# Performance work log

Hardware: AMD Instinct MI355X
Metric: run time of the kernel (lower is better)

The kernel has to match this reference:

```python
import jax, jax.numpy as jnp
from jax import lax
import numpy as np
import math

B, C, Hs, Ws = 2, 512, 48, 48
HW = Hs * Ws            # 2304; also m (compress_ratio = 1)
M = HW
GROUPS = 256
GS = M // GROUPS        # 9, exact split
ALPHA = 0.05
MAXITER = 43
TOL = B * HW * 1e-7     # torch: z0.numel()*tol with z0 of shape [N, HW]
EPS = 1e-5
POWER_ITERS = 100


def _make_A():
    # random projection: num_ones = round(sqrt(m)) ones per column, rows L2-normalized
    rng = np.random.RandomState(0)
    num_ones = int(round(math.sqrt(M)))  # 48
    A = np.zeros((M, HW), dtype=np.float32)
    rows = np.argsort(rng.rand(HW, M), axis=1)[:, :num_ones]  # [HW, num_ones]
    A[rows.ravel(), np.repeat(np.arange(HW), num_ones)] = 1.0
    A /= np.maximum(np.sqrt((A ** 2).sum(axis=1, keepdims=True)), 1e-12)
    return jnp.asarray(A)


def setup_inputs() -> dict:
    key = jax.random.key(0)
    ks = jax.random.split(key, 10)
    f32 = jnp.float32
    d = {
        'content': jax.random.normal(ks[0], (B, C, Hs, Ws), f32),
        'style': jax.random.normal(ks[1], (B, C, Hs, Ws), f32),
        'content_key': jax.random.normal(ks[2], (B, C, Hs, Ws), f32),
        'style_key': jax.random.normal(ks[3], (B, C, Hs, Ws), f32),
        'f_w': jax.random.normal(ks[4], (C, C), f32) * 0.02,
        'f_b': jnp.zeros((C,), f32),
        'g_w': jax.random.normal(ks[5], (C, C), f32) * 0.02,
        'g_b': jnp.zeros((C,), f32),
        'h_w': jax.random.normal(ks[6], (C, C), f32) * 0.02,
        'h_b': jnp.zeros((C,), f32),
        'A': _make_A(),
    }
    return d


def _conv1x1(x, w, b):
    # nn.Conv2d(Cin, Cout, 1): [b,c,h,w] x [o,c] + bias
    return jnp.einsum('bchw,oc->bohw', x, w) + b[None, :, None, None]


def _softshrink(x, lam):
    return jnp.sign(x) * jnp.maximum(jnp.abs(x) - lam, 0.0)


def _forward(content, style, content_key, style_key, f_w, f_b, g_w, g_b, h_w, h_b, A):
    Fq = _conv1x1(content_key, f_w, f_b).reshape(B, C, HW).transpose(0, 2, 1)  # [b,HWc,Ck]
    G = _conv1x1(style_key, g_w, g_b).reshape(B, C, HW)                        # [b,Ck,HWs]
    Hh = _conv1x1(style, h_w, h_b).reshape(B, C, HW)
    # HW <= max_sample: no subsampling branch
    style_flat = Hh.transpose(0, 2, 1)                                         # [b,HWs,C]
    S = jax.nn.softmax(jnp.einsum('bqc,bck->bqk', Fq, G), axis=-1)             # [b,HWc,HWs]
    mean = jnp.einsum('bqk,bkc->bqc', S, style_flat)                           # weighted mean
    std = jnp.sqrt(jax.nn.relu(jnp.einsum('bqk,bkc->bqc', S, style_flat ** 2) - mean ** 2))
    mean = mean.transpose(0, 2, 1)  # [b,C,HW]
    std = std.transpose(0, 2, 1)
    # random projection along spatial dim: feat @ A^T
    proj = lambda f: jnp.einsum('mh,bch->bcm', A, f)
    mean_c = proj(mean)
    std_c = proj(std)
    cont_c = proj(content.reshape(B, C, HW))
    # per-group mean/variance norm (256 equal groups of GS along compressed dim)
    g = cont_c.reshape(B, C, GROUPS, GS)
    mu = g.mean(axis=-1, keepdims=True)
    var = g.var(axis=-1, ddof=1, keepdims=True)  # torch var is unbiased
    normed = (g - mu) / jnp.sqrt(var + EPS)
    x = (normed * std_c.reshape(B, C, GROUPS, GS)
         + mean_c.reshape(B, C, GROUPS, GS)).reshape(B, C, M)
    # FISTA sparse coding: min 0.5||z A^T - x||^2 + alpha |z|_1
    Ad = lax.stop_gradient(A)
    WtW = Ad.T @ Ad
    v = jnp.full((HW,), 1.0 / math.sqrt(HW), jnp.float32)
    def _pi(v, _):
        w = WtW @ v
        return w / jnp.linalg.norm(w), None
    v, _ = lax.scan(_pi, v, None, length=POWER_ITERS)
    L = v @ (WtW @ v)  # largest eigenvalue of A^T A
    lr = 1.0 / L
    z0 = jnp.zeros((B, C, HW), x.dtype)

    def step(carry, _):
        z, y, t, done = carry
        resid = jnp.einsum('bch,mh->bcm', y, A) - x   # y @ A^T - x
        grad = jnp.einsum('bcm,mh->bch', resid, A)    # resid @ A
        zn = _softshrink(y - lr * grad, ALPHA * lr)
        diff = jnp.abs(z - zn).sum()
        tn = (1.0 + jnp.sqrt(1.0 + 4.0 * t * t)) / 2.0
        yn = zn + (t - 1.0) / tn * (zn - z)
        z2 = jnp.where(done, z, zn)
        y2 = jnp.where(done, y, yn)
        t2 = jnp.where(done, t, tn)
        done2 = done | (diff <= TOL)
        return (z2, y2, t2, done2), None

    (z, _, _, _), _ = lax.scan(step, (z0, z0, jnp.float32(1.0), jnp.array(False)),
                               None, length=MAXITER)
    return z.reshape(B, C, Hs, Ws)


def reference(content, style, content_key, style_key, f_w, f_b, g_w, g_b, h_w, h_b, A):
    return _forward(content, style, content_key, style_key,
                    f_w, f_b, g_w, g_b, h_w, h_b, A)
```

## Files before the change

### kernel.cpp

```cpp
#include <hip/hip_runtime.h>
#include <math.h>

#define TPB 256

typedef _Float16 f16;
typedef _Float16 half8 __attribute__((ext_vector_type(8)));
typedef _Float16 f16x2 __attribute__((ext_vector_type(2)));
typedef _Float16 f16x4 __attribute__((ext_vector_type(4)));
typedef float floatx4 __attribute__((ext_vector_type(4)));

static constexpr int CDIM = 512;
static constexpr int HWD = 2304;
static constexpr float ALPHA = 0.05f;
static constexpr float TOLF = 4.608e-4f;

enum { EPI_F32 = 0, EPI_F16BIASN = 1, EPI_F16BIASM = 2, EPI_F16 = 3,
       EPI_WTW = 4, EPI_MEANSTD = 5, EPI_FISTA = 6 };

__device__ __forceinline__ bool fista_done(const float* __restrict__ diffArr, int iter) {
    bool done = false;
    for (int j = 0; j < iter; ++j) done = done || (diffArr[j] <= TOLF);
    return done;
}

__device__ __forceinline__ void gload_lds(const f16* g, f16* l) {
#if __has_builtin(__builtin_amdgcn_global_load_lds)
    __builtin_amdgcn_global_load_lds(
        (__attribute__((address_space(1))) void*)(g),
        (__attribute__((address_space(3))) void*)(l), 16, 0, 0);
#else
    *(int4*)l = *(const int4*)g;
#endif
}

template<int N> __device__ __forceinline__ void vwait() {
    if constexpr (N == 0)      asm volatile("s_waitcnt vmcnt(0)" ::: "memory");
    else if constexpr (N == 3) asm volatile("s_waitcnt vmcnt(3)" ::: "memory");
    else if constexpr (N == 4) asm volatile("s_waitcnt vmcnt(4)" ::: "memory");
}

__device__ __forceinline__ void barrier_f() {
    asm volatile("" ::: "memory");
    __builtin_amdgcn_s_barrier();
    asm volatile("" ::: "memory");
}

template<int EPI, int MF>
__global__ __launch_bounds__(TPB, 4) void sgemm(
    const f16* __restrict__ A, long a_bs, int lda,
    const f16* __restrict__ B, long b_bs, int ldb,
    void* __restrict__ C0, long c_bs, int ldc,
    void* __restrict__ C1,
    int K,
    const float* __restrict__ bias,
    const float* __restrict__ xAf,
    float* __restrict__ zc, float* __restrict__ zp, f16* __restrict__ yhp,
    const float* __restrict__ lrs, float coefPrev, float coefCur,
    float* __restrict__ diffArr, int iter)
{
    if (EPI == EPI_FISTA) {
        if (iter > 0 && fista_done(diffArr, iter)) return;
    }
    constexpr int ASZ = MF * 32 * 64;
    constexpr int BSZ = 64 * 64;
    constexpr int LCNT = MF + 2;
    __shared__ alignas(16) f16 As[2 * ASZ];
    __shared__ alignas(16) f16 Bs[2 * BSZ];
    const int tid = threadIdx.x;
    const int wid = tid >> 6, lane = tid & 63;
    const int wr = wid >> 1, wc = wid & 1;

    const int gx = gridDim.x, gy = gridDim.y;
    const int nwg = gx * gy;
    const int d = blockIdx.y * gx + blockIdx.x;
    const int q = nwg >> 3, r = nwg & 7;
    const int xcd = d & 7, rest = d >> 3;
    const int wgid = (xcd < r ? xcd * (q + 1) : r * (q + 1) + (xcd - r) * q) + rest;
    const int bx = wgid / gy, by = wgid % gy;

    const int m0 = by * (MF * 32), n0 = bx << 6;
    const f16* Ab = A + (long)blockIdx.z * a_bs;
    const f16* Bb = B + (long)blockIdx.z * b_bs;

    floatx4 acc[MF][2] = {};
    floatx4 acc2[MF][2] = {};

    const int rl = lane & 15, kg = lane >> 4;
    const int lrow = lane >> 3;
    const int gs = (lane & 7) ^ lrow;

    const int nt = K >> 6;

    auto STAGE = [&](int t, int buf) {
        const long k0 = (long)t << 6;
        f16* Ad = As + buf * ASZ;
        f16* Bd = Bs + buf * BSZ;
        #pragma unroll
        for (int p = 0; p < MF; ++p) {
            const int c = wid * MF + p;
            const int R = c * 8 + lrow;
            gload_lds(Ab + (long)(m0 + R) * lda + k0 + gs * 8, Ad + c * 512);
        }
        #pragma unroll
        for (int p = 0; p < 2; ++p) {
            const int c = wid * 2 + p;
            const int R = c * 8 + lrow;
            gload_lds(Bb + (long)(n0 + R) * ldb + k0 + gs * 8, Bd + c * 512);
        }
    };

    STAGE(0, 0);
    for (int t = 0; t < nt; ++t) {
        if (t + 1 < nt) {
            STAGE(t + 1, (t + 1) & 1);
            vwait<LCNT>();
        } else {
            vwait<0>();
        }
        barrier_f();
        const f16* Ac = As + (t & 1) * ASZ;
        const f16* Bc = Bs + (t & 1) * BSZ;
        #pragma unroll
        for (int kk = 0; kk < 2; ++kk) {
            const int j = kk * 4 + kg;
            half8 af[MF], bf[2];
            #pragma unroll
            for (int f = 0; f < MF; ++f) {
                const int rowa = wr * (MF * 16) + f * 16 + rl;
                af[f] = *(const half8*)&Ac[rowa * 64 + ((j ^ (rowa & 7)) * 8)];
            }
            #pragma unroll
            for (int f = 0; f < 2; ++f) {
                const int rowb = wc * 32 + f * 16 + rl;
                bf[f] = *(const half8*)&Bc[rowb * 64 + ((j ^ (rowb & 7)) * 8)];
            }
            #pragma unroll
            for (int fi = 0; fi < MF; ++fi) {
                #pragma unroll
                for (int fj = 0; fj < 2; ++fj) {
                    acc[fi][fj] = __builtin_amdgcn_mfma_f32_16x16x32_f16(af[fi], bf[fj], acc[fi][fj], 0, 0, 0);
                    if constexpr (EPI == EPI_MEANSTD) {
                        half8 bq = bf[fj] * bf[fj];
                        acc2[fi][fj] = __builtin_amdgcn_mfma_f32_16x16x32_f16(af[fi], bq, acc2[fi][fj], 0, 0, 0);
                    }
                }
            }
        }
        barrier_f();
    }

    const int rg = lane >> 4;
    const int bz = blockIdx.z;
    float loc = 0.f;
    float lr = 0.f, sh = 0.f;
    if constexpr (EPI == EPI_FISTA) { lr = lrs[0]; sh = lrs[1]; }

    #pragma unroll
    for (int fi = 0; fi < MF; ++fi) {
        #pragma unroll
        for (int fj = 0; fj < 2; ++fj) {
            #pragma unroll
            for (int r2 = 0; r2 < 4; ++r2) {
                const int row = m0 + wr * (MF * 16) + fi * 16 + rg * 4 + r2;
                const int col = n0 + wc * 32 + fj * 16 + rl;
                const float v = acc[fi][fj][r2];
                if constexpr (EPI == EPI_F32) {
                    ((float*)C0)[bz * c_bs + (long)row * ldc + col] = v;
                } else if constexpr (EPI == EPI_F16BIASN) {
                    ((f16*)C0)[bz * c_bs + (long)row * ldc + col] = (f16)(v + bias[col]);
                } else if constexpr (EPI == EPI_F16BIASM) {
                    ((f16*)C0)[bz * c_bs + (long)row * ldc + col] = (f16)(v + bias[row]);
                } else if constexpr (EPI == EPI_F16) {
                    ((f16*)C0)[bz * c_bs + (long)row * ldc + col] = (f16)v;
                } else if constexpr (EPI == EPI_WTW) {
                    ((float*)C0)[(long)row * ldc + col] = v;
                    ((f16*)C1)[(long)row * ldc + col] = (f16)v;
                } else if constexpr (EPI == EPI_MEANSTD) {
                    const float m_ = v;
                    float s2 = acc2[fi][fj][r2] - m_ * m_;
                    const long o = ((long)bz * CDIM + col) * HWD + row;
                    ((f16*)C0)[o] = (f16)m_;
                    ((f16*)C1)[o] = (f16)sqrtf(s2 > 0.f ? s2 : 0.f);
                } else {
                    const long off = (long)row * HWD + col;
                    const float zk = zc[off];
                    const float zkm = zp[off];
                    const float ykf = zk + coefPrev * (zk - zkm);
                    const float grad = v - xAf[off];
                    const float p = ykf - lr * grad;
                    const float ap = fabsf(p) - sh;
                    const float zn = ap > 0.f ? copysignf(ap, p) : 0.f;
                    zp[off] = zn;
                    yhp[off] = (f16)(zn + coefCur * (zn - zk));
                    loc += fabsf(zn - zk);
                }
            }
        }
    }
    if constexpr (EPI == EPI_FISTA) {
        __shared__ float red[TPB];
        red[tid] = loc; __syncthreads();
        for (int s = 128; s > 0; s >>= 1) { if (tid < s) red[tid] += red[tid + s]; __syncthreads(); }
        if (tid == 0) atomicAdd(&diffArr[iter], red[0]);
    }
}

__global__ __launch_bounds__(TPB) void tcvt(const float* __restrict__ in, long in_bs,
                                            f16* __restrict__ out, long out_bs, int R, int Cc) {
    __shared__ float t[32][33];
    const int b = blockIdx.z;
    const int r0 = blockIdx.y << 5, c0 = blockIdx.x << 5;
    const int tx = threadIdx.x & 31, ty = threadIdx.x >> 5;
    const float* ib = in + (long)b * in_bs;
    #pragma unroll
    for (int p = 0; p < 4; ++p) {
        const int r = ty + p * 8;
        t[r][tx] = ib[(long)(r0 + r) * Cc + c0 + tx];
    }
    __syncthreads();
    f16* ob = out + (long)b * out_bs;
    #pragma unroll
    for (int p = 0; p < 4; ++p) {
        const int c = ty + p * 8;
        ob[(long)(c0 + c) * R + r0 + tx] = (f16)t[tx][c];
    }
}

__global__ void cvt16(const float4* __restrict__ in, f16x4* __restrict__ out, long n4) {
    long i = (long)blockIdx.x * blockDim.x + threadIdx.x;
    const long st = (long)gridDim.x * blockDim.x;
    for (; i < n4; i += st) {
        const float4 v = in[i];
        f16x4 o; o.x = (f16)v.x; o.y = (f16)v.y; o.z = (f16)v.z; o.w = (f16)v.w;
        out[i] = o;
    }
}

__global__ __launch_bounds__(TPB) void softmax_h(const float* __restrict__ Sf, f16* __restrict__ Sh) {
    __shared__ float row[HWD];
    __shared__ float red[TPB];
    const long base = (long)blockIdx.x * HWD;
    const int tid = threadIdx.x;
    float mx = -3.4e38f;
    for (int i = tid; i < HWD; i += TPB) { const float v = Sf[base + i]; row[i] = v; mx = fmaxf(mx, v); }
    red[tid] = mx; __syncthreads();
    for (int s = 128; s > 0; s >>= 1) { if (tid < s) red[tid] = fmaxf(red[tid], red[tid + s]); __syncthreads(); }
    mx = red[0]; __syncthreads();
    float sum = 0.f;
    for (int i = tid; i < HWD; i += TPB) { const float e = expf(row[i] - mx); row[i] = e; sum += e; }
    red[tid] = sum; __syncthreads();
    for (int s = 128; s > 0; s >>= 1) { if (tid < s) red[tid] += red[tid + s]; __syncthreads(); }
    const float inv = 1.0f / red[0];
    for (int i = tid; i < HWD; i += TPB) Sh[base + i] = (f16)(row[i] * inv);
}

__global__ __launch_bounds__(TPB) void groupnorm_x(const float* __restrict__ contc,
                                                   const float* __restrict__ meanc,
                                                   const float* __restrict__ stdc,
                                                   f16* __restrict__ xh) {
    const long base = (long)blockIdx.x * HWD + (long)threadIdx.x * 9;
    float v[9];
    float mu = 0.f;
    #pragma unroll
    for (int j = 0; j < 9; ++j) { v[j] = contc[base + j]; mu += v[j]; }
    mu *= (1.0f / 9.0f);
    float var = 0.f;
    #pragma unroll
    for (int j = 0; j < 9; ++j) { const float d = v[j] - mu; var += d * d; }
    var *= (1.0f / 8.0f);
    const float rs = 1.0f / sqrtf(var + 1e-5f);
    #pragma unroll
    for (int j = 0; j < 9; ++j)
        xh[base + j] = (f16)((v[j] - mu) * rs * (float)stdc[base + j] + (float)meanc[base + j]);
}

__global__ __launch_bounds__(TPB) void matvec_h(const f16* __restrict__ Wm,
                                                const float* __restrict__ win,
                                                float* __restrict__ wout) {
    __shared__ float red[TPB];
    const int tid = threadIdx.x;
    float s = 0.f;
    for (int i = tid; i < HWD; i += TPB) { const float v = win[i]; s += v * v; }
    red[tid] = s; __syncthreads();
    for (int st = 128; st > 0; st >>= 1) { if (tid < st) red[tid] += red[tid + st]; __syncthreads(); }
    const float ninv = rsqrtf(red[0]);
    const int row = (blockIdx.x << 2) + (tid >> 6);
    const int lane = tid & 63;
    const f16x2* wr2 = (const f16x2*)(Wm + (long)row * HWD);
    float d = 0.f;
    for (int j = lane; j < HWD / 2; j += 64) {
        const f16x2 p = wr2[j];
        d += (float)p.x * win[2 * j] + (float)p.y * win[2 * j + 1];
    }
    #pragma unroll
    for (int o = 32; o > 0; o >>= 1) d += __shfl_down(d, o);
    if (lane == 0) wout[row] = d * ninv;
}

__global__ __launch_bounds__(TPB) void kernelL(const float* __restrict__ Wf,
                                               const float* __restrict__ w,
                                               float* __restrict__ Lnum, float* __restrict__ Lden) {
    __shared__ float red[TPB];
    const int tid = threadIdx.x;
    const int row = (blockIdx.x << 2) + (tid >> 6);
    const int lane = tid & 63;
    const float* wr = Wf + (long)row * HWD;
    float d = 0.f;
    for (int j = lane; j < HWD; j += 64) d += wr[j] * w[j];
    #pragma unroll
    for (int o = 32; o > 0; o >>= 1) d += __shfl_down(d, o);
    red[tid] = (lane == 0) ? d * w[row] : 0.f;
    __syncthreads();
    for (int s = 128; s > 0; s >>= 1) { if (tid < s) red[tid] += red[tid + s]; __syncthreads(); }
    if (tid == 0) atomicAdd(Lnum, red[0]);
    if (blockIdx.x == 0) {
        __syncthreads();
        float s2 = 0.f;
        for (int i = tid; i < HWD; i += TPB) { const float v = w[i]; s2 += v * v; }
        red[tid] = s2; __syncthreads();
        for (int s = 128; s > 0; s >>= 1) { if (tid < s) red[tid] += red[tid + s]; __syncthreads(); }
        if (tid == 0) *Lden = red[0];
    }
}

__global__ void lr_fin(const float* __restrict__ Lnum, const float* __restrict__ Lden,
                       float* __restrict__ lrs) {
    const float lr = Lden[0] / Lnum[0];
    lrs[0] = lr;
    lrs[1] = ALPHA * lr;
}

__global__ void init_small(float* __restrict__ wvec, float* __restrict__ diffArr,
                           float* __restrict__ Lnum) {
    const int tid = threadIdx.x;
    for (int i = tid; i < HWD; i += TPB) wvec[i] = (float)(1.0 / 48.0);
    if (tid < 43) diffArr[tid] = 0.f;
    if (tid == 64) Lnum[0] = 0.f;
}

__global__ void zero_kernel(float4* __restrict__ p, long n4) {
    long i = (long)blockIdx.x * blockDim.x + threadIdx.x;
    const long st = (long)gridDim.x * blockDim.x;
    for (; i < n4; i += st) p[i] = make_float4(0.f, 0.f, 0.f, 0.f);
}

__global__ void copy_fista(const float4* __restrict__ zfA, const float4* __restrict__ zfB,
                           float4* __restrict__ out, const float* __restrict__ diffArr, long n4) {
    int last = 42;
    for (int j = 0; j < 43; ++j) { if (diffArr[j] <= TOLF) { last = j; break; } }
    const float4* src = (last & 1) ? zfA : zfB;
    long i = (long)blockIdx.x * blockDim.x + threadIdx.x;
    const long st = (long)gridDim.x * blockDim.x;
    for (; i < n4; i += st) out[i] = src[i];
}

extern "C" void kernel_launch(void* const* d_in, const int* in_sizes, int n_in,
                              void* d_out, int out_size, void* d_ws, size_t ws_size,
                              hipStream_t stream) {
    (void)in_sizes; (void)n_in; (void)out_size;
    const float* content = (const float*)d_in[0];
    const float* style   = (const float*)d_in[1];
    const float* ckey    = (const float*)d_in[2];
    const float* skey    = (const float*)d_in[3];
    const float* f_w = (const float*)d_in[4];
    const float* f_b = (const float*)d_in[5];
    const float* g_w = (const float*)d_in[6];
    const float* g_b = (const float*)d_in[7];
    const float* h_w = (const float*)d_in[8];
    const float* h_b = (const float*)d_in[9];
    const float* Amat = (const float*)d_in[10];

    if (ws_size < 79500000) return;
    char* W = (char*)d_ws;

    const long E16 = (long)HWD * CDIM;
    const long EHH = (long)HWD * HWD;
    f16*  ckeyT = (f16*)(W + 0);
    f16*  skeyT = (f16*)(W + 4718592);
    f16*  styleT= (f16*)(W + 9437184);
    float* Sf   = (float*)(W + 0);
    f16*  Ah    = (f16*)(W + 0);
    f16*  At    = (f16*)(W + 10616832);
    f16*  Wh    = (f16*)(W + 21233664);
    f16*  W4h   = (f16*)(W + 31850496);
    f16*  W2h   = (f16*)(W + 0);
    float* contc= (float*)(W + 21233664);
    float* zfA  = (float*)(W + 0);
    float* zfB  = (float*)(W + 9437184);
    f16*  yh    = (f16*)(W + 31850496);
    f16*  Sh    = (f16*)(W + 42467328);
    float* meanc= (float*)(W + 42467328);
    float* stdc = (float*)(W + 42467328 + 9437184);
    float* Wf   = (float*)(W + 42467328);
    float* xAf  = (float*)(W + 42467328);
    f16*  Fh    = (f16*)(W + 63700992);
    f16*  Gh    = (f16*)(W + 63700992 + 4718592);
    f16*  Hh    = (f16*)(W + 63700992 + 9437184);
    f16*  meanx = (f16*)(W + 63700992);
    f16*  stdx  = (f16*)(W + 63700992 + 4718592);
    f16*  conth = (f16*)(W + 63700992 + 9437184);
    f16*  xh    = (f16*)(W + 63700992);
    float* w_a  = (float*)(W + 77856768);
    float* w_b  = (float*)(W + 77856768 + 9216);
    float* lrs  = (float*)(W + 77856768 + 18432);
    float* Lnum = (float*)(W + 77856768 + 18440);
    float* Lden = (float*)(W + 77856768 + 18444);
    float* diffArr = (float*)(W + 77856768 + 18448);
    f16*  fwh   = (f16*)(W + 77875712);
    f16*  gwh   = (f16*)(W + 77875712 + 524288);
    f16*  hwh   = (f16*)(W + 77875712 + 1048576);

    init_small<<<1, TPB, 0, stream>>>(w_a, diffArr, Lnum);

    cvt16<<<256, TPB, 0, stream>>>((const float4*)f_w, (f16x4*)fwh, (long)CDIM * CDIM / 4);
    cvt16<<<256, TPB, 0, stream>>>((const float4*)g_w, (f16x4*)gwh, (long)CDIM * CDIM / 4);
    cvt16<<<256, TPB, 0, stream>>>((const float4*)h_w, (f16x4*)hwh, (long)CDIM * CDIM / 4);
    tcvt<<<dim3(72, 16, 2), TPB, 0, stream>>>(ckey, E16, ckeyT, E16, CDIM, HWD);
    tcvt<<<dim3(72, 16, 2), TPB, 0, stream>>>(skey, E16, skeyT, E16, CDIM, HWD);
    tcvt<<<dim3(72, 16, 2), TPB, 0, stream>>>(style, E16, styleT, E16, CDIM, HWD);

    sgemm<EPI_F16BIASN, 1><<<dim3(8, 72, 2), TPB, 0, stream>>>(ckeyT, E16, CDIM, fwh, 0, CDIM,
        Fh, E16, CDIM, nullptr, CDIM, f_b, nullptr, nullptr, nullptr, nullptr, nullptr, 0.f, 0.f, nullptr, 0);
    sgemm<EPI_F16BIASN, 1><<<dim3(8, 72, 2), TPB, 0, stream>>>(skeyT, E16, CDIM, gwh, 0, CDIM,
        Gh, E16, CDIM, nullptr, CDIM, g_b, nullptr, nullptr, nullptr, nullptr, nullptr, 0.f, 0.f, nullptr, 0);
    sgemm<EPI_F16BIASM, 1><<<dim3(36, 16, 2), TPB, 0, stream>>>(hwh, 0, CDIM, styleT, E16, CDIM,
        Hh, E16, HWD, nullptr, CDIM, h_b, nullptr, nullptr, nullptr, nullptr, nullptr, 0.f, 0.f, nullptr, 0);

    sgemm<EPI_F32, 2><<<dim3(36, 36, 2), TPB, 0, stream>>>(Fh, E16, CDIM, Gh, E16, CDIM,
        Sf, EHH, HWD, nullptr, CDIM, nullptr, nullptr, nullptr, nullptr, nullptr, nullptr, 0.f, 0.f, nullptr, 0);
    softmax_h<<<2 * HWD, TPB, 0, stream>>>(Sf, Sh);

    cvt16<<<2048, TPB, 0, stream>>>((const float4*)Amat, (f16x4*)Ah, EHH / 4);
    tcvt<<<dim3(72, 72, 1), TPB, 0, stream>>>(Amat, 0, At, 0, HWD, HWD);

    sgemm<EPI_MEANSTD, 1><<<dim3(8, 72, 2), TPB, 0, stream>>>(Sh, EHH, HWD, Hh, E16, HWD,
        meanx, 0, HWD, stdx, HWD, nullptr, nullptr, nullptr, nullptr, nullptr, nullptr, 0.f, 0.f, nullptr, 0);

    cvt16<<<2048, TPB, 0, stream>>>((const float4*)content, (f16x4*)conth, (long)2 * E16 / 4);

    sgemm<EPI_F32, 1><<<dim3(36, 32, 1), TPB, 0, stream>>>(meanx, 0, HWD, Ah, 0, HWD,
        meanc, 0, HWD, nullptr, HWD, nullptr, nullptr, nullptr, nullptr, nullptr, nullptr, 0.f, 0.f, nullptr, 0);
    sgemm<EPI_F32, 1><<<dim3(36, 32, 1), TPB, 0, stream>>>(stdx, 0, HWD, Ah, 0, HWD,
        stdc, 0, HWD, nullptr, HWD, nullptr, nullptr, nullptr, nullptr, nullptr, nullptr, 0.f, 0.f, nullptr, 0);
    sgemm<EPI_F32, 1><<<dim3(36, 32, 1), TPB, 0, stream>>>(conth, 0, HWD, Ah, 0, HWD,
        contc, 0, HWD, nullptr, HWD, nullptr, nullptr, nullptr, nullptr, nullptr, nullptr, 0.f, 0.f, nullptr, 0);

    groupnorm_x<<<1024, TPB, 0, stream>>>(contc, meanc, stdc, xh);

    sgemm<EPI_WTW, 2><<<dim3(36, 36, 1), TPB, 0, stream>>>(At, 0, HWD, At, 0, HWD,
        Wf, 0, HWD, Wh, HWD, nullptr, nullptr, nullptr, nullptr, nullptr, nullptr, 0.f, 0.f, nullptr, 0);
    sgemm<EPI_F16, 2><<<dim3(36, 36, 1), TPB, 0, stream>>>(Wh, 0, HWD, Wh, 0, HWD,
        W2h, 0, HWD, nullptr, HWD, nullptr, nullptr, nullptr, nullptr, nullptr, nullptr, 0.f, 0.f, nullptr, 0);
    sgemm<EPI_F16, 2><<<dim3(36, 36, 1), TPB, 0, stream>>>(W2h, 0, HWD, W2h, 0, HWD,
        W4h, 0, HWD, nullptr, HWD, nullptr, nullptr, nullptr, nullptr, nullptr, nullptr, 0.f, 0.f, nullptr, 0);

    for (int it = 0; it < 25; ++it) {
        const float* win = (it & 1) ? w_b : w_a;
        float* wout = (it & 1) ? w_a : w_b;
        matvec_h<<<HWD / 4, TPB, 0, stream>>>(W4h, win, wout);
    }
    kernelL<<<HWD / 4, TPB, 0, stream>>>(Wf, w_b, Lnum, Lden);
    lr_fin<<<1, 1, 0, stream>>>(Lnum, Lden, lrs);

    sgemm<EPI_F32, 1><<<dim3(36, 32, 1), TPB, 0, stream>>>(xh, 0, HWD, At, 0, HWD,
        xAf, 0, HWD, nullptr, HWD, nullptr, nullptr, nullptr, nullptr, nullptr, nullptr, 0.f, 0.f, nullptr, 0);

    zero_kernel<<<1024, TPB, 0, stream>>>((float4*)zfA, E16);
    zero_kernel<<<1024, TPB, 0, stream>>>((float4*)yh, E16 / 4);

    float t = 1.0f, coefPrev = 0.0f;
    for (int it = 0; it < 43; ++it) {
        const float tn = (1.0f + sqrtf(1.0f + 4.0f * t * t)) * 0.5f;
        const float coef = (t - 1.0f) / tn;
        t = tn;
        float* zc = (it & 1) ? zfB : zfA;
        float* zp = (it & 1) ? zfA : zfB;
        sgemm<EPI_FISTA, 1><<<dim3(36, 32, 1), TPB, 0, stream>>>(yh, 0, HWD, Wh, 0, HWD,
            nullptr, 0, HWD, nullptr, HWD, nullptr, xAf, zc, zp, yh, lrs, coefPrev, coef, diffArr, it);
        coefPrev = coef;
    }

    copy_fista<<<2048, TPB, 0, stream>>>((const float4*)zfA, (const float4*)zfB,
                                         (float4*)d_out, diffArr, 2 * E16 / 4);
}
```

Baseline: 2.423 ms.

## Run FISTA loop as one persistent cooperative kernel with register-resident state

Replaces the 43 separate FISTA GEMM launches with a single cooperative persistent kernel. It keeps z, y and xA in registers, ping-pongs y between two fp16 buffers, and uses a grid-wide sync plus an atomic diff sum for early exit. The aim is to remove launch overhead and the z/zp global-memory traffic each iteration. Other GEMMs move to larger M tiles (MF=2) to cut launch counts and reuse B tiles. The change adds grid.sync cost and relies on all 288 blocks being co-resident, falling back to a per-step kernel otherwise.

```diff
diff --git a/kernel.cpp b/kernel.cpp
--- a/kernel.cpp
+++ b/kernel.cpp
@@ -1,5 +1,8 @@
 #include <hip/hip_runtime.h>
+#include <hip/hip_cooperative_groups.h>
 #include <math.h>
+
+namespace cg = cooperative_groups;
 
 #define TPB 256
 
@@ -15,7 +18,7 @@
 static constexpr float TOLF = 4.608e-4f;
 
 enum { EPI_F32 = 0, EPI_F16BIASN = 1, EPI_F16BIASM = 2, EPI_F16 = 3,
-       EPI_WTW = 4, EPI_MEANSTD = 5, EPI_FISTA = 6 };
+       EPI_WTW = 4, EPI_MEANSTD = 5 };
 
 __device__ __forceinline__ bool fista_done(const float* __restrict__ diffArr, int iter) {
     bool done = false;
@@ -35,8 +38,8 @@
 
 template<int N> __device__ __forceinline__ void vwait() {
     if constexpr (N == 0)      asm volatile("s_waitcnt vmcnt(0)" ::: "memory");
-    else if constexpr (N == 3) asm volatile("s_waitcnt vmcnt(3)" ::: "memory");
     else if constexpr (N == 4) asm volatile("s_waitcnt vmcnt(4)" ::: "memory");
+    else if constexpr (N == 6) asm volatile("s_waitcnt vmcnt(6)" ::: "memory");
 }
 
 __device__ __forceinline__ void barrier_f() {
@@ -52,15 +55,8 @@
     void* __restrict__ C0, long c_bs, int ldc,
     void* __restrict__ C1,
     int K,
-    const float* __restrict__ bias,
-    const float* __restrict__ xAf,
-    float* __restrict__ zc, float* __restrict__ zp, f16* __restrict__ yhp,
-    const float* __restrict__ lrs, float coefPrev, float coefCur,
-    float* __restrict__ diffArr, int iter)
+    const float* __restrict__ bias)
 {
-    if (EPI == EPI_FISTA) {
-        if (iter > 0 && fista_done(diffArr, iter)) return;
-    }
     constexpr int ASZ = MF * 32 * 64;
     constexpr int BSZ = 64 * 64;
     constexpr int LCNT = MF + 2;
@@ -88,7 +84,6 @@
     const int rl = lane & 15, kg = lane >> 4;
     const int lrow = lane >> 3;
     const int gs = (lane & 7) ^ lrow;
-
     const int nt = K >> 6;
 
     auto STAGE = [&](int t, int buf) {
@@ -111,12 +106,8 @@
 
     STAGE(0, 0);
     for (int t = 0; t < nt; ++t) {
-        if (t + 1 < nt) {
-            STAGE(t + 1, (t + 1) & 1);
-            vwait<LCNT>();
-        } else {
-            vwait<0>();
-        }
+        if (t + 1 < nt) { STAGE(t + 1, (t + 1) & 1); vwait<LCNT>(); }
+        else            { vwait<0>(); }
         barrier_f();
         const f16* Ac = As + (t & 1) * ASZ;
         const f16* Bc = Bs + (t & 1) * BSZ;
@@ -151,10 +142,6 @@
 
     const int rg = lane >> 4;
     const int bz = blockIdx.z;
-    float loc = 0.f;
-    float lr = 0.f, sh = 0.f;
-    if constexpr (EPI == EPI_FISTA) { lr = lrs[0]; sh = lrs[1]; }
-
     #pragma unroll
     for (int fi = 0; fi < MF; ++fi) {
         #pragma unroll
@@ -181,28 +168,262 @@
                     const long o = ((long)bz * CDIM + col) * HWD + row;
                     ((f16*)C0)[o] = (f16)m_;
                     ((f16*)C1)[o] = (f16)sqrtf(s2 > 0.f ? s2 : 0.f);
-                } else {
-                    const long off = (long)row * HWD + col;
-                    const float zk = zc[off];
-                    const float zkm = zp[off];
-                    const float ykf = zk + coefPrev * (zk - zkm);
-                    const float grad = v - xAf[off];
-                    const float p = ykf - lr * grad;
+                }
+            }
+        }
+    }
+}
+
+__global__ __launch_bounds__(TPB, 2) void fista_coop(
+    const f16* __restrict__ Wh,
+    const float* __restrict__ xAf,
+    f16* __restrict__ yA, f16* __restrict__ yB,
+    const float* __restrict__ lrs,
+    float* __restrict__ diffArr,
+    float* __restrict__ dout)
+{
+    cg::grid_group grid = cg::this_grid();
+    constexpr int MF = 4;
+    constexpr int ASZ = MF * 32 * 64;
+    constexpr int BSZ = 64 * 64;
+    constexpr int LCNT = MF + 2;
+    __shared__ alignas(16) f16 As[2 * ASZ];
+    __shared__ alignas(16) f16 Bs[2 * BSZ];
+    __shared__ float red[TPB];
+    const int tid = threadIdx.x;
+    const int wid = tid >> 6, lane = tid & 63;
+    const int wr = wid >> 1, wc = wid & 1;
+
+    const int d = blockIdx.x;
+    const int wgid = (d & 7) * 36 + (d >> 3);
+    const int bx = wgid >> 3, by = wgid & 7;
+    const int m0 = by << 7, n0 = bx << 6;
+
+    const int rl = lane & 15, kg = lane >> 4;
+    const int rg = lane >> 4;
+    const int lrow = lane >> 3;
+    const int gs = (lane & 7) ^ lrow;
+    constexpr int nt = HWD >> 6;
+
+    const float lr = lrs[0], sh = lrs[1];
+
+    float xar[MF][2][4], zr[MF][2][4], yr[MF][2][4];
+    #pragma unroll
+    for (int fi = 0; fi < MF; ++fi)
+        #pragma unroll
+        for (int fj = 0; fj < 2; ++fj)
+            #pragma unroll
+            for (int r2 = 0; r2 < 4; ++r2) {
+                const int row = m0 + wr * (MF * 16) + fi * 16 + rg * 4 + r2;
+                const int col = n0 + wc * 32 + fj * 16 + rl;
+                xar[fi][fj][r2] = xAf[(long)row * HWD + col];
+                zr[fi][fj][r2] = 0.f;
+                yr[fi][fj][r2] = 0.f;
+            }
+
+    float t = 1.0f;
+    for (int iter = 0; iter < 43; ++iter) {
+        const float tn = (1.0f + sqrtf(1.0f + 4.0f * t * t)) * 0.5f;
+        const float coef = (t - 1.0f) / tn;
+        t = tn;
+        const f16* Yin = (iter & 1) ? yB : yA;
+        f16* Yout = (iter & 1) ? yA : yB;
+
+        floatx4 acc[MF][2] = {};
+        auto STAGE = [&](int tt, int buf) {
+            const long k0 = (long)tt << 6;
+            f16* Ad = As + buf * ASZ;
+            f16* Bd = Bs + buf * BSZ;
+            #pragma unroll
+            for (int p = 0; p < MF; ++p) {
+                const int c = wid * MF + p;
+                const int R = c * 8 + lrow;
+                gload_lds(Yin + (long)(m0 + R) * HWD + k0 + gs * 8, Ad + c * 512);
+            }
+            #pragma unroll
+            for (int p = 0; p < 2; ++p) {
+                const int c = wid * 2 + p;
+                const int R = c * 8 + lrow;
+                gload_lds(Wh + (long)(n0 + R) * HWD + k0 + gs * 8, Bd + c * 512);
+            }
+        };
+        STAGE(0, 0);
+        for (int tt = 0; tt < nt; ++tt) {
+            if (tt + 1 < nt) { STAGE(tt + 1, (tt + 1) & 1); vwait<LCNT>(); }
+            else             { vwait<0>(); }
+            barrier_f();
+            const f16* Ac = As + (tt & 1) * ASZ;
+            const f16* Bc = Bs + (tt & 1) * BSZ;
+            #pragma unroll
+            for (int kk = 0; kk < 2; ++kk) {
+                const int j = kk * 4 + kg;
+                half8 af[MF], bf[2];
+                #pragma unroll
+                for (int f = 0; f < MF; ++f) {
+                    const int rowa = wr * (MF * 16) + f * 16 + rl;
+                    af[f] = *(const half8*)&Ac[rowa * 64 + ((j ^ (rowa & 7)) * 8)];
+                }
+                #pragma unroll
+                for (int f = 0; f < 2; ++f) {
+                    const int rowb = wc * 32 + f * 16 + rl;
+                    bf[f] = *(const half8*)&Bc[rowb * 64 + ((j ^ (rowb & 7)) * 8)];
+                }
+                #pragma unroll
+                for (int fi = 0; fi < MF; ++fi)
+                    #pragma unroll
+                    for (int fj = 0; fj < 2; ++fj)
+                        acc[fi][fj] = __builtin_amdgcn_mfma_f32_16x16x32_f16(af[fi], bf[fj], acc[fi][fj], 0, 0, 0);
+            }
+            barrier_f();
+        }
+
+        float loc = 0.f;
+        #pragma unroll
+        for (int fi = 0; fi < MF; ++fi)
+            #pragma unroll
+            for (int fj = 0; fj < 2; ++fj)
+                #pragma unroll
+                for (int r2 = 0; r2 < 4; ++r2) {
+                    const int row = m0 + wr * (MF * 16) + fi * 16 + rg * 4 + r2;
+                    const int col = n0 + wc * 32 + fj * 16 + rl;
+                    const float grad = acc[fi][fj][r2] - xar[fi][fj][r2];
+                    const float p = yr[fi][fj][r2] - lr * grad;
                     const float ap = fabsf(p) - sh;
                     const float zn = ap > 0.f ? copysignf(ap, p) : 0.f;
-                    zp[off] = zn;
-                    yhp[off] = (f16)(zn + coefCur * (zn - zk));
-                    loc += fabsf(zn - zk);
+                    const float zo = zr[fi][fj][r2];
+                    loc += fabsf(zn - zo);
+                    const float yn = zn + coef * (zn - zo);
+                    zr[fi][fj][r2] = zn;
+                    yr[fi][fj][r2] = yn;
+                    Yout[(long)row * HWD + col] = (f16)yn;
                 }
-            }
-        }
-    }
-    if constexpr (EPI == EPI_FISTA) {
-        __shared__ float red[TPB];
         red[tid] = loc; __syncthreads();
         for (int s = 128; s > 0; s >>= 1) { if (tid < s) red[tid] += red[tid + s]; __syncthreads(); }
         if (tid == 0) atomicAdd(&diffArr[iter], red[0]);
-    }
+
+        __threadfence();
+        grid.sync();
+        __threadfence();
+        const float dsum = __hip_atomic_load(&diffArr[iter], __ATOMIC_RELAXED,
+                                             __HIP_MEMORY_SCOPE_AGENT);
+        if (dsum <= TOLF) break;
+    }
+
+    #pragma unroll
+    for (int fi = 0; fi < MF; ++fi)
+        #pragma unroll
+        for (int fj = 0; fj < 2; ++fj)
+            #pragma unroll
+            for (int r2 = 0; r2 < 4; ++r2) {
+                const int row = m0 + wr * (MF * 16) + fi * 16 + rg * 4 + r2;
+                const int col = n0 + wc * 32 + fj * 16 + rl;
+                dout[(long)row * HWD + col] = zr[fi][fj][r2];
+            }
+}
+
+__global__ __launch_bounds__(TPB, 3) void fista_step(
+    const f16* __restrict__ Yin, const f16* __restrict__ Wh,
+    const float* __restrict__ xAf,
+    float* __restrict__ zc, float* __restrict__ zp, f16* __restrict__ yhp,
+    const float* __restrict__ lrs, float coefPrev, float coefCur,
+    float* __restrict__ diffArr, int iter)
+{
+    if (iter > 0 && fista_done(diffArr, iter)) return;
+    constexpr int MF = 2;
+    constexpr int ASZ = MF * 32 * 64;
+    constexpr int BSZ = 64 * 64;
+    constexpr int LCNT = MF + 2;
+    __shared__ alignas(16) f16 As[2 * ASZ];
+    __shared__ alignas(16) f16 Bs[2 * BSZ];
+    __shared__ float red[TPB];
+    const int tid = threadIdx.x;
+    const int wid = tid >> 6, lane = tid & 63;
+    const int wr = wid >> 1, wc = wid & 1;
+
+    const int d = blockIdx.y * gridDim.x + blockIdx.x;
+    const int wgid = (d & 7) * 72 + (d >> 3);
+    const int bx = wgid >> 4, by = wgid & 15;
+    const int m0 = by << 6, n0 = bx << 6;
+
+    floatx4 acc[MF][2] = {};
+    const int rl = lane & 15, kg = lane >> 4;
+    const int lrow = lane >> 3;
+    const int gs = (lane & 7) ^ lrow;
+    constexpr int nt = HWD >> 6;
+
+    auto STAGE = [&](int t, int buf) {
+        const long k0 = (long)t << 6;
+        f16* Ad = As + buf * ASZ;
+        f16* Bd = Bs + buf * BSZ;
+        #pragma unroll
+        for (int p = 0; p < MF; ++p) {
+            const int c = wid * MF + p;
+            const int R = c * 8 + lrow;
+            gload_lds(Yin + (long)(m0 + R) * HWD + k0 + gs * 8, Ad + c * 512);
+        }
+        #pragma unroll
+        for (int p = 0; p < 2; ++p) {
+            const int c = wid * 2 + p;
+            const int R = c * 8 + lrow;
+            gload_lds(Wh + (long)(n0 + R) * HWD + k0 + gs * 8, Bd + c * 512);
+        }
+    };
+    STAGE(0, 0);
+    for (int t = 0; t < nt; ++t) {
+        if (t + 1 < nt) { STAGE(t + 1, (t + 1) & 1); vwait<LCNT>(); }
+        else            { vwait<0>(); }
+        barrier_f();
+        const f16* Ac = As + (t & 1) * ASZ;
+        const f16* Bc = Bs + (t & 1) * BSZ;
+        #pragma unroll
+        for (int kk = 0; kk < 2; ++kk) {
+            const int j = kk * 4 + kg;
+            half8 af[MF], bf[2];
+            #pragma unroll
+            for (int f = 0; f < MF; ++f) {
+                const int rowa = wr * (MF * 16) + f * 16 + rl;
+                af[f] = *(const half8*)&Ac[rowa * 64 + ((j ^ (rowa & 7)) * 8)];
+            }
+            #pragma unroll
+            for (int f = 0; f < 2; ++f) {
+                const int rowb = wc * 32 + f * 16 + rl;
+                bf[f] = *(const half8*)&Bc[rowb * 64 + ((j ^ (rowb & 7)) * 8)];
+            }
+            #pragma unroll
+            for (int fi = 0; fi < MF; ++fi)
+                #pragma unroll
+                for (int fj = 0; fj < 2; ++fj)
+                    acc[fi][fj] = __builtin_amdgcn_mfma_f32_16x16x32_f16(af[fi], bf[fj], acc[fi][fj], 0, 0, 0);
+        }
+        barrier_f();
+    }
+
+    const int rg = lane >> 4;
+    const float lr = lrs[0], sh = lrs[1];
+    float loc = 0.f;
+    #pragma unroll
+    for (int fi = 0; fi < MF; ++fi)
+        #pragma unroll
+        for (int fj = 0; fj < 2; ++fj)
+            #pragma unroll
+            for (int r2 = 0; r2 < 4; ++r2) {
+                const int row = m0 + wr * (MF * 16) + fi * 16 + rg * 4 + r2;
+                const int col = n0 + wc * 32 + fj * 16 + rl;
+                const long off = (long)row * HWD + col;
+                const float zk = zc[off];
+                const float zkm = zp[off];
+                const float ykf = zk + coefPrev * (zk - zkm);
+                const float grad = acc[fi][fj][r2] - xAf[off];
+                const float p = ykf - lr * grad;
+                const float ap = fabsf(p) - sh;
+                const float zn = ap > 0.f ? copysignf(ap, p) : 0.f;
+                zp[off] = zn;
+                yhp[off] = (f16)(zn + coefCur * (zn - zk));
+                loc += fabsf(zn - zk);
+            }
+    red[tid] = loc; __syncthreads();
+    for (int s = 128; s > 0; s >>= 1) { if (tid < s) red[tid] += red[tid + s]; __syncthreads(); }
+    if (tid == 0) atomicAdd(&diffArr[iter], red[0]);
 }
 
 __global__ __launch_bounds__(TPB) void tcvt(const float* __restrict__ in, long in_bs,
@@ -387,7 +608,8 @@
     float* contc= (float*)(W + 21233664);
     float* zfA  = (float*)(W + 0);
     float* zfB  = (float*)(W + 9437184);
-    f16*  yh    = (f16*)(W + 31850496);
+    f16*  yhA   = (f16*)(W + 31850496);
+    f16*  yhB   = (f16*)(W + 36569088);
     f16*  Sh    = (f16*)(W + 42467328);
     float* meanc= (float*)(W + 42467328);
     float* stdc = (float*)(W + 42467328 + 9437184);
@@ -419,40 +641,40 @@
     tcvt<<<dim3(72, 16, 2), TPB, 0, stream>>>(skey, E16, skeyT, E16, CDIM, HWD);
     tcvt<<<dim3(72, 16, 2), TPB, 0, stream>>>(style, E16, styleT, E16, CDIM, HWD);
 
-    sgemm<EPI_F16BIASN, 1><<<dim3(8, 72, 2), TPB, 0, stream>>>(ckeyT, E16, CDIM, fwh, 0, CDIM,
-        Fh, E16, CDIM, nullptr, CDIM, f_b, nullptr, nullptr, nullptr, nullptr, nullptr, 0.f, 0.f, nullptr, 0);
-    sgemm<EPI_F16BIASN, 1><<<dim3(8, 72, 2), TPB, 0, stream>>>(skeyT, E16, CDIM, gwh, 0, CDIM,
-        Gh, E16, CDIM, nullptr, CDIM, g_b, nullptr, nullptr, nullptr, nullptr, nullptr, 0.f, 0.f, nullptr, 0);
-    sgemm<EPI_F16BIASM, 1><<<dim3(36, 16, 2), TPB, 0, stream>>>(hwh, 0, CDIM, styleT, E16, CDIM,
-        Hh, E16, HWD, nullptr, CDIM, h_b, nullptr, nullptr, nullptr, nullptr, nullptr, 0.f, 0.f, nullptr, 0);
+    sgemm<EPI_F16BIASN, 2><<<dim3(8, 36, 2), TPB, 0, stream>>>(ckeyT, E16, CDIM, fwh, 0, CDIM,
+        Fh, E16, CDIM, nullptr, CDIM, f_b);
+    sgemm<EPI_F16BIASN, 2><<<dim3(8, 36, 2), TPB, 0, stream>>>(skeyT, E16, CDIM, gwh, 0, CDIM,
+        Gh, E16, CDIM, nullptr, CDIM, g_b);
+    sgemm<EPI_F16BIASM, 2><<<dim3(36, 8, 2), TPB, 0, stream>>>(hwh, 0, CDIM, styleT, E16, CDIM,
+        Hh, E16, HWD, nullptr, CDIM, h_b);
 
     sgemm<EPI_F32, 2><<<dim3(36, 36, 2), TPB, 0, stream>>>(Fh, E16, CDIM, Gh, E16, CDIM,
-        Sf, EHH, HWD, nullptr, CDIM, nullptr, nullptr, nullptr, nullptr, nullptr, nullptr, 0.f, 0.f, nullptr, 0);
+        Sf, EHH, HWD, nullptr, CDIM, nullptr);
     softmax_h<<<2 * HWD, TPB, 0, stream>>>(Sf, Sh);
 
     cvt16<<<2048, TPB, 0, stream>>>((const float4*)Amat, (f16x4*)Ah, EHH / 4);
     tcvt<<<dim3(72, 72, 1), TPB, 0, stream>>>(Amat, 0, At, 0, HWD, HWD);
 
-    sgemm<EPI_MEANSTD, 1><<<dim3(8, 72, 2), TPB, 0, stream>>>(Sh, EHH, HWD, Hh, E16, HWD,
-        meanx, 0, HWD, stdx, HWD, nullptr, nullptr, nullptr, nullptr, nullptr, nullptr, 0.f, 0.f, nullptr, 0);
+    sgemm<EPI_MEANSTD, 2><<<dim3(8, 36, 2), TPB, 0, stream>>>(Sh, EHH, HWD, Hh, E16, HWD,
+        meanx, 0, HWD, stdx, HWD, nullptr);
 
     cvt16<<<2048, TPB, 0, stream>>>((const float4*)content, (f16x4*)conth, (long)2 * E16 / 4);
 
-    sgemm<EPI_F32, 1><<<dim3(36, 32, 1), TPB, 0, stream>>>(meanx, 0, HWD, Ah, 0, HWD,
-        meanc, 0, HWD, nullptr, HWD, nullptr, nullptr, nullptr, nullptr, nullptr, nullptr, 0.f, 0.f, nullptr, 0);
-    sgemm<EPI_F32, 1><<<dim3(36, 32, 1), TPB, 0, stream>>>(stdx, 0, HWD, Ah, 0, HWD,
-        stdc, 0, HWD, nullptr, HWD, nullptr, nullptr, nullptr, nullptr, nullptr, nullptr, 0.f, 0.f, nullptr, 0);
-    sgemm<EPI_F32, 1><<<dim3(36, 32, 1), TPB, 0, stream>>>(conth, 0, HWD, Ah, 0, HWD,
-        contc, 0, HWD, nullptr, HWD, nullptr, nullptr, nullptr, nullptr, nullptr, nullptr, 0.f, 0.f, nullptr, 0);
+    sgemm<EPI_F32, 2><<<dim3(36, 16, 1), TPB, 0, stream>>>(meanx, 0, HWD, Ah, 0, HWD,
+        meanc, 0, HWD, nullptr, HWD, nullptr);
+    sgemm<EPI_F32, 2><<<dim3(36, 16, 1), TPB, 0, stream>>>(stdx, 0, HWD, Ah, 0, HWD,
+        stdc, 0, HWD, nullptr, HWD, nullptr);
+    sgemm<EPI_F32, 2><<<dim3(36, 16, 1), TPB, 0, stream>>>(conth, 0, HWD, Ah, 0, HWD,
+        contc, 0, HWD, nullptr, HWD, nullptr);
 
     groupnorm_x<<<1024, TPB, 0, stream>>>(contc, meanc, stdc, xh);
 
     sgemm<EPI_WTW, 2><<<dim3(36, 36, 1), TPB, 0, stream>>>(At, 0, HWD, At, 0, HWD,
-        Wf, 0, HWD, Wh, HWD, nullptr, nullptr, nullptr, nullptr, nullptr, nullptr, 0.f, 0.f, nullptr, 0);
+        Wf, 0, HWD, Wh, HWD, nullptr);
     sgemm<EPI_F16, 2><<<dim3(36, 36, 1), TPB, 0, stream>>>(Wh, 0, HWD, Wh, 0, HWD,
-        W2h, 0, HWD, nullptr, HWD, nullptr, nullptr, nullptr, nullptr, nullptr, nullptr, 0.f, 0.f, nullptr, 0);
+        W2h, 0, HWD, nullptr, HWD, nullptr);
     sgemm<EPI_F16, 2><<<dim3(36, 36, 1), TPB, 0, stream>>>(W2h, 0, HWD, W2h, 0, HWD,
-        W4h, 0, HWD, nullptr, HWD, nullptr, nullptr, nullptr, nullptr, nullptr, nullptr, 0.f, 0.f, nullptr, 0);
+        W4h, 0, HWD, nullptr, HWD, nullptr);
 
     for (int it = 0; it < 25; ++it) {
         const float* win = (it & 1) ? w_b : w_a;
@@ -462,24 +684,38 @@
     kernelL<<<HWD / 4, TPB, 0, stream>>>(Wf, w_b, Lnum, Lden);
     lr_fin<<<1, 1, 0, stream>>>(Lnum, Lden, lrs);
 
-    sgemm<EPI_F32, 1><<<dim3(36, 32, 1), TPB, 0, stream>>>(xh, 0, HWD, At, 0, HWD,
-        xAf, 0, HWD, nullptr, HWD, nullptr, nullptr, nullptr, nullptr, nullptr, nullptr, 0.f, 0.f, nullptr, 0);
-
-    zero_kernel<<<1024, TPB, 0, stream>>>((float4*)zfA, E16);
-    zero_kernel<<<1024, TPB, 0, stream>>>((float4*)yh, E16 / 4);
-
-    float t = 1.0f, coefPrev = 0.0f;
-    for (int it = 0; it < 43; ++it) {
-        const float tn = (1.0f + sqrtf(1.0f + 4.0f * t * t)) * 0.5f;
-        const float coef = (t - 1.0f) / tn;
-        t = tn;
-        float* zc = (it & 1) ? zfB : zfA;
-        float* zp = (it & 1) ? zfA : zfB;
-        sgemm<EPI_FISTA, 1><<<dim3(36, 32, 1), TPB, 0, stream>>>(yh, 0, HWD, Wh, 0, HWD,
-            nullptr, 0, HWD, nullptr, HWD, nullptr, xAf, zc, zp, yh, lrs, coefPrev, coef, diffArr, it);
-        coefPrev = coef;
-    }
-
-    copy_fista<<<2048, TPB, 0, stream>>>((const float4*)zfA, (const float4*)zfB,
-                                         (float4*)d_out, diffArr, 2 * E16 / 4);
-}
+    sgemm<EPI_F32, 2><<<dim3(36, 16, 1), TPB, 0, stream>>>(xh, 0, HWD, At, 0, HWD,
+        xAf, 0, HWD, nullptr, HWD, nullptr);
+
+    int dev = 0; hipGetDevice(&dev);
+    int coopOK = 0, numCU = 0, maxB = 0;
+    hipDeviceGetAttribute(&coopOK, hipDeviceAttributeCooperativeLaunch, dev);
+    hipDeviceGetAttribute(&numCU, hipDeviceAttributeMultiprocessorCount, dev);
+    hipOccupancyMaxActiveBlocksPerMultiprocessor(&maxB, fista_coop, TPB, 0);
+    const bool useCoop = coopOK && ((long)maxB * numCU >= 288);
+
+    zero_kernel<<<1024, TPB, 0, stream>>>((float4*)yhA, E16 / 4);
+
+    if (useCoop) {
+        float* doutF = (float*)d_out;
+        void* args[] = { (void*)&Wh, (void*)&xAf, (void*)&yhA, (void*)&yhB,
+                         (void*)&lrs, (void*)&diffArr, (void*)&doutF };
+        hipLaunchCooperativeKernel((const void*)fista_coop, dim3(288), dim3(TPB),
+                                   args, 0, stream);
+    } else {
+        zero_kernel<<<1024, TPB, 0, stream>>>((float4*)zfA, E16);
+        float t = 1.0f, coefPrev = 0.0f;
+        for (int it = 0; it < 43; ++it) {
+            const float tn = (1.0f + sqrtf(1.0f + 4.0f * t * t)) * 0.5f;
+            const float coef = (t - 1.0f) / tn;
+            t = tn;
+            float* zc = (it & 1) ? zfB : zfA;
+            float* zp = (it & 1) ? zfA : zfB;
+            fista_step<<<dim3(36, 16, 1), TPB, 0, stream>>>(yhA, Wh, xAf, zc, zp, yhA,
+                                                            lrs, coefPrev, coef, diffArr, it);
+            coefPrev = coef;
+        }
+        copy_fista<<<2048, TPB, 0, stream>>>((const float4*)zfA, (const float4*)zfB,
+                                             (float4*)d_out, diffArr, 2 * E16 / 4);
+    }
+}
```

Result: faster. 2.112 ms (-12.8%).
